# Optimization experiments

Measured on AMD Instinct MI355X. Metric: run time of the kernel, lower is better.

## Reference

```python
import jax, jax.numpy as jnp
import numpy as np

N = 100_000   # nodes
E = 200_000   # directed edges
G = 2_500     # graphs in batch
F_NODE = 16
F_EDGE = 8
H1 = 32
H2 = 16


def setup_inputs() -> dict:
    key = jax.random.key(0)
    ks = jax.random.split(key, 24)
    p = lambda k, shape: 0.1 * jax.random.normal(k, shape, dtype=jnp.float32)
    inp = {
        "x": jax.random.normal(ks[0], (N, F_NODE), dtype=jnp.float32),
        "edge_attr": jax.random.normal(ks[1], (E, F_EDGE), dtype=jnp.float32),
        # edge-MLP for conv1: F_EDGE -> 16 -> F_NODE*H1
        "w_e1a": p(ks[2], (F_EDGE, 16)), "b_e1a": p(ks[3], (16,)),
        "w_e1b": p(ks[4], (16, F_NODE * H1)), "b_e1b": p(ks[5], (F_NODE * H1,)),
        "w_root1": p(ks[6], (F_NODE, H1)), "b_root1": p(ks[7], (H1,)),
        # edge-MLP for conv2: F_EDGE -> 16 -> H1*H2
        "w_e2a": p(ks[8], (F_EDGE, 16)), "b_e2a": p(ks[9], (16,)),
        "w_e2b": p(ks[10], (16, H1 * H2)), "b_e2b": p(ks[11], (H1 * H2,)),
        "w_root2": p(ks[12], (H1, H2)), "b_root2": p(ks[13], (H2,)),
        # attention-pool gate nn: F_NODE -> F_NODE -> 1
        "w_g1": p(ks[14], (F_NODE, F_NODE)), "b_g1": p(ks[15], (F_NODE,)),
        "w_g2": p(ks[16], (F_NODE, 1)), "b_g2": p(ks[17], (1,)),
        # head: (H2 + F_NODE) -> 8 -> 1
        "w_l1": p(ks[18], (H2 + F_NODE, 8)), "b_l1": p(ks[19], (8,)),
        "w_l2": p(ks[20], (8, 1)), "b_l2": p(ks[21], (1,)),
        "edge_index": jax.random.randint(ks[22], (2, E), 0, N),
        "batch": jnp.sort(jax.random.randint(ks[23], (N,), 0, G)),
    }
    return inp


def _nnconv(x, src, tgt, edge_attr, wa, ba, wb, bb, wr, br, in_c, out_c, n):
    # PyG NNConv: x_i' = x_i @ W_root + b + sum_{j->i} x_j @ Theta(e_ji)
    h = jax.nn.relu(edge_attr @ wa + ba)              # [E, 16]
    theta = (h @ wb + bb).reshape(-1, in_c, out_c)    # [E, in, out]
    msg = jnp.einsum('ei,eio->eo', x[src], theta)     # [E, out]
    agg = jax.ops.segment_sum(msg, tgt, num_segments=n)
    return x @ wr + br + agg


def reference(x, edge_attr, w_e1a, b_e1a, w_e1b, b_e1b, w_root1, b_root1,
              w_e2a, b_e2a, w_e2b, b_e2b, w_root2, b_root2,
              w_g1, b_g1, w_g2, b_g2, w_l1, b_l1, w_l2, b_l2,
              edge_index, batch):
    src, tgt = edge_index[0], edge_index[1]
    n = x.shape[0]

    # GlobalAttention pooling on raw node features (per-graph segment softmax)
    gate = jax.nn.relu(x @ w_g1 + b_g1) @ w_g2 + b_g2          # [N, 1]
    m = jax.ops.segment_max(gate, batch, num_segments=G)       # [G, 1]
    a = jnp.exp(gate - m[batch])
    s = jax.ops.segment_sum(a, batch, num_segments=G)
    x_att = jax.ops.segment_sum((a / s[batch]) * x, batch, num_segments=G)  # [G, F_NODE]

    # Two NNConv layers with ReLU
    h = jax.nn.relu(_nnconv(x, src, tgt, edge_attr, w_e1a, b_e1a, w_e1b, b_e1b,
                            w_root1, b_root1, F_NODE, H1, n))
    h = jax.nn.relu(_nnconv(h, src, tgt, edge_attr, w_e2a, b_e2a, w_e2b, b_e2b,
                            w_root2, b_root2, H1, H2, n))

    # global_mean_pool
    cnt = jax.ops.segment_sum(jnp.ones((n, 1), h.dtype), batch, num_segments=G)
    mean = jax.ops.segment_sum(h, batch, num_segments=G) / jnp.maximum(cnt, 1.0)

    z = jnp.concatenate([mean, x_att], axis=1)  # [G, H2 + F_NODE]
    # eval mode: dropout p=0.5 is identity; two linear layers, no activation between
    z = z @ w_l1 + b_l1
    z = z @ w_l2 + b_l2
    return z
```

## Files before the change

kernel.cpp:

```cpp
#include <hip/hip_runtime.h>
#include <hip/hip_bf16.h>

#define NN 100000
#define NE 200000
#define NG 2500
#define FN 16
#define FE 8
#define H1C 32
#define H2C 16
#define KH 16

typedef __attribute__((ext_vector_type(8))) short short8;
typedef __attribute__((ext_vector_type(4))) float f32x4;
typedef _Float16 __attribute__((ext_vector_type(2))) half2v;
typedef _Float16 __attribute__((ext_vector_type(8))) half8v;
typedef __fp16 __attribute__((ext_vector_type(2))) pkf16x2;

__device__ __forceinline__ float bf2f(unsigned int u){
  union { unsigned int i; float f; } v; v.i = (u & 0xffffu) << 16; return v.f;
}
__device__ __forceinline__ unsigned int pkh(float a, float b){
  union { pkf16x2 h; unsigned int u; } v; v.h = __builtin_amdgcn_cvt_pkrtz(a, b); return v.u;
}
__device__ __forceinline__ unsigned short f2h(float f){
  union { _Float16 h; unsigned short s; } v; v.h = (_Float16)f; return v.s;
}
__device__ __forceinline__ float h2lo(unsigned int u){
  union { unsigned short s; _Float16 h; } v; v.s = (unsigned short)u; return (float)v.h;
}
__device__ __forceinline__ float h2hi(unsigned int u){
  union { unsigned short s; _Float16 h; } v; v.s = (unsigned short)(u >> 16); return (float)v.h;
}
__device__ __forceinline__ float rdf(const void* p, long i, bool isbf){
  return isbf ? bf2f(((const unsigned short*)p)[i]) : ((const float*)p)[i];
}
__device__ __forceinline__ bool detect_isbf(const void* __restrict__ x){
  const unsigned short* u = (const unsigned short*)x;
  int lane = threadIdx.x & 63;
  float f = bf2f(u[2*lane]);
  float a = fabsf(f);
  bool sane = (f == 0.0f) || (a > 1e-4f && a < 1e4f);
  unsigned long long b = __ballot(sane);
  return __popcll(b) >= 32;
}

#define NW 20
struct WArgs { const void* p[NW]; };
enum {
  OW_E1A=0,     OB_E1A=128,   OW_E1B=144,   OB_E1B=8336,  OW_R1=8848,  OB_R1=9360,
  OW_E2A=9392,  OB_E2A=9520,  OW_E2B=9536,  OB_E2B=17728, OW_R2=18240, OB_R2=18752,
  OW_G1=18768,  OB_G1=19024,  OW_G2=19040,  OB_G2=19056,
  OW_L1=19057,  OB_L1=19313,  OW_L2=19321,  OB_L2=19329
};

#define MB_A 76
#define MB_B (MB_A + 19)
#define MB_C (MB_B + 18)
#define MB_D (MB_C + 391)
#define MB_E (MB_D + 782)
__global__ void __launch_bounds__(256) mega1_kernel(
    const void* __restrict__ xin, const void* __restrict__ efin, WArgs w,
    const int* __restrict__ ei, const int* __restrict__ batch,
    float* __restrict__ wts, unsigned int* __restrict__ wpack1, unsigned int* __restrict__ wpack2,
    float* __restrict__ gate, float* __restrict__ xf, int* __restrict__ deg,
    int* __restrict__ gstart)
{
  int b = blockIdx.x, tid = threadIdx.x;
  if(b < MB_A){
    bool isbf = detect_isbf(xin);
    int i = b*256 + tid;
    if(i >= 19330) return;
    const int sz[NW] = {128,16,8192,512,512,32, 128,16,8192,512,512,16, 256,16,16,1, 256,8,8,1};
    int seg = 0; long base = 0;
    while(i - base >= sz[seg]){ base += sz[seg]; seg++; }
    wts[i] = rdf(w.p[seg], i - base, isbf);
    return;
  }
  if(b < MB_B){
    bool isbf = detect_isbf(xin);
    int j = (b - MB_A)*256 + tid;
    if(j >= 4736) return;
    int n = j / 148; int k = (j % 148) * 2;
    float v0 = 0.f, v1 = 0.f;
    if(k < 256)        v0 = rdf(w.p[2], (long)k*32 + n, isbf);
    else if(k < 272)   v0 = rdf(w.p[3], (long)(k-256)*32 + n, isbf);
    if(k+1 < 256)      v1 = rdf(w.p[2], (long)(k+1)*32 + n, isbf);
    else if(k+1 < 272) v1 = rdf(w.p[3], (long)(k+1-256)*32 + n, isbf);
    wpack1[j] = pkh(v0, v1);
    return;
  }
  if(b < MB_C){
    bool isbf = detect_isbf(xin);
    int j = (b - MB_B)*256 + tid;
    if(j >= 4416) return;
    int n = j / 276; int k = (j % 276) * 2;
    float v0 = 0.f, v1 = 0.f;
    if(k < 512)        v0 = rdf(w.p[8], (long)k*16 + n, isbf);
    else if(k < 544)   v0 = rdf(w.p[9], (long)(k-512)*16 + n, isbf);
    if(k+1 < 512)      v1 = rdf(w.p[8], (long)(k+1)*16 + n, isbf);
    else if(k+1 < 544) v1 = rdf(w.p[9], (long)(k+1-512)*16 + n, isbf);
    wpack2[j] = pkh(v0, v1);
    return;
  }
  if(b < MB_D){
    __shared__ float s_w1[FN*FN], s_b1[FN], s_w2[FN], s_b2v[1];
    bool isbf = detect_isbf(xin);
    if(tid < FN*FN) s_w1[tid] = rdf(w.p[12], tid, isbf);
    if(tid < FN){ s_b1[tid] = rdf(w.p[13], tid, isbf); s_w2[tid] = rdf(w.p[14], tid, isbf); }
    if(tid == 0) s_b2v[0] = rdf(w.p[15], 0, isbf);
    __syncthreads();
    int n = (b - MB_C)*256 + tid;
    if(n >= NN) return;
    {
      int b1 = batch[n];
      int b0 = (n == 0) ? -1 : batch[n-1];
      for(int g2 = b0 + 1; g2 <= b1; g2++) gstart[g2] = n;
      if(n == NN-1) for(int g2 = b1 + 1; g2 <= NG; g2++) gstart[g2] = NN;
    }
    float xv[FN];
    if(isbf){
      uint4 u0 = ((const uint4*)xin)[2*n], u1 = ((const uint4*)xin)[2*n+1];
      xv[0]=bf2f(u0.x); xv[1]=bf2f(u0.x>>16); xv[2]=bf2f(u0.y); xv[3]=bf2f(u0.y>>16);
      xv[4]=bf2f(u0.z); xv[5]=bf2f(u0.z>>16); xv[6]=bf2f(u0.w); xv[7]=bf2f(u0.w>>16);
      xv[8]=bf2f(u1.x); xv[9]=bf2f(u1.x>>16); xv[10]=bf2f(u1.y); xv[11]=bf2f(u1.y>>16);
      xv[12]=bf2f(u1.z); xv[13]=bf2f(u1.z>>16); xv[14]=bf2f(u1.w); xv[15]=bf2f(u1.w>>16);
    } else {
      #pragma unroll
      for(int q = 0; q < 4; q++){
        float4 v = ((const float4*)xin)[4*n + q];
        xv[q*4+0]=v.x; xv[q*4+1]=v.y; xv[q*4+2]=v.z; xv[q*4+3]=v.w;
      }
    }
    float4* xo = (float4*)(xf + (size_t)n*FN);
    #pragma unroll
    for(int q = 0; q < 4; q++) xo[q] = make_float4(xv[q*4+0], xv[q*4+1], xv[q*4+2], xv[q*4+3]);
    float g = s_b2v[0];
    #pragma unroll
    for(int j = 0; j < FN; j++){
      float hj = s_b1[j];
      #pragma unroll
      for(int i = 0; i < FN; i++) hj += xv[i] * s_w1[i*FN + j];
      hj = hj > 0.f ? hj : 0.f;
      g += hj * s_w2[j];
    }
    gate[n] = g;
    return;
  }
  {
    int e = (b - MB_D)*256 + tid;
    if(e < NE) atomicAdd(&deg[ei[NE + e]], 1);
  }
}

#define SCAN_NB 98
__global__ void __launch_bounds__(256) scan_kernel(
    const int* __restrict__ deg, int* __restrict__ rowptr, int* __restrict__ cursor,
    unsigned int* __restrict__ pub)
{
  __shared__ int s_thr[256];
  __shared__ int s_agg[SCAN_NB];
  __shared__ int s_bcast;
  int tid = threadIdx.x, bid = blockIdx.x;
  int base = bid*1024 + tid*4;
  int v0=0, v1=0, v2=0, v3=0;
  if(base + 3 < NN){
    int4 t4 = *(const int4*)(deg + base);
    v0=t4.x; v1=t4.y; v2=t4.z; v3=t4.w;
  } else {
    if(base+0 < NN) v0 = deg[base+0];
    if(base+1 < NN) v1 = deg[base+1];
    if(base+2 < NN) v2 = deg[base+2];
  }
  int e1 = v0, e2 = v0+v1, e3 = v0+v1+v2, tot = v0+v1+v2+v3;
  s_thr[tid] = tot;
  __syncthreads();
  for(int off = 1; off < 256; off <<= 1){
    int t = (tid >= off) ? s_thr[tid-off] : 0;
    __syncthreads();
    s_thr[tid] += t;
    __syncthreads();
  }
  int thr_excl = s_thr[tid] - tot;
  int agg = s_thr[255];
  if(tid == 0) atomicExch(&pub[bid], ((unsigned int)agg << 1) | 1u);
  if(tid < SCAN_NB){
    unsigned int v;
    do { v = atomicAdd(&pub[tid], 0u); } while((v & 1u) == 0u);
    s_agg[tid] = (int)(v >> 1);
  }
  __syncthreads();
  if(tid == 0){
    int acc = 0;
    for(int p = 0; p < bid; p++) acc += s_agg[p];
    s_bcast = acc;
  }
  __syncthreads();
  int ex = s_bcast + thr_excl;
  if(base + 3 < NN){
    int4 r = make_int4(ex, ex+e1, ex+e2, ex+e3);
    *(int4*)(rowptr + base) = r;
    *(int4*)(cursor + base) = r;
  } else {
    if(base+0 < NN){ rowptr[base+0]=ex;    cursor[base+0]=ex;    }
    if(base+1 < NN){ rowptr[base+1]=ex+e1; cursor[base+1]=ex+e1; }
    if(base+2 < NN){ rowptr[base+2]=ex+e2; cursor[base+2]=ex+e2; }
  }
  if(bid == 0 && tid == 0) rowptr[NN] = NE;
}

__global__ void __launch_bounds__(256) fill_edge_kernel(
    const int* __restrict__ ei, int* __restrict__ cursor,
    const void* __restrict__ efin, const float* __restrict__ wts, const void* __restrict__ xin,
    int* __restrict__ srcp, unsigned int* __restrict__ hpk1, unsigned int* __restrict__ hpk2)
{
  __shared__ float s_w1[FE*KH], s_b1[KH], s_w2[FE*KH], s_b2[KH];
  int tid = threadIdx.x;
  if(tid < FE*KH){ s_w1[tid] = wts[OW_E1A + tid]; s_w2[tid] = wts[OW_E2A + tid]; }
  if(tid < KH){ s_b1[tid] = wts[OB_E1A + tid]; s_b2[tid] = wts[OB_E2A + tid]; }
  bool isbf = detect_isbf(xin);
  __syncthreads();
  int e = blockIdx.x*256 + tid;
  if(e >= NE) return;
  int pos = atomicAdd(&cursor[ei[NE + e]], 1);
  srcp[pos] = ei[e];
  float ev[FE];
  if(isbf){
    uint4 u = ((const uint4*)efin)[e];
    ev[0]=bf2f(u.x); ev[1]=bf2f(u.x>>16); ev[2]=bf2f(u.y); ev[3]=bf2f(u.y>>16);
    ev[4]=bf2f(u.z); ev[5]=bf2f(u.z>>16); ev[6]=bf2f(u.w); ev[7]=bf2f(u.w>>16);
  } else {
    float4 a = ((const float4*)efin)[2*e], b = ((const float4*)efin)[2*e+1];
    ev[0]=a.x; ev[1]=a.y; ev[2]=a.z; ev[3]=a.w; ev[4]=b.x; ev[5]=b.y; ev[6]=b.z; ev[7]=b.w;
  }
  unsigned int o[8];
  #pragma unroll
  for(int d = 0; d < 8; d++){
    float h0 = s_b1[2*d], h1 = s_b1[2*d+1];
    #pragma unroll
    for(int k = 0; k < FE; k++){
      h0 += ev[k] * s_w1[k*KH + 2*d];
      h1 += ev[k] * s_w1[k*KH + 2*d+1];
    }
    h0 = h0 > 0.f ? h0 : 0.f; h1 = h1 > 0.f ? h1 : 0.f;
    o[d] = pkh(h0, h1);
  }
  uint4* p1 = (uint4*)(hpk1 + (size_t)pos*8);
  p1[0] = make_uint4(o[0],o[1],o[2],o[3]); p1[1] = make_uint4(o[4],o[5],o[6],o[7]);
  #pragma unroll
  for(int d = 0; d < 8; d++){
    float h0 = s_b2[2*d], h1 = s_b2[2*d+1];
    #pragma unroll
    for(int k = 0; k < FE; k++){
      h0 += ev[k] * s_w2[k*KH + 2*d];
      h1 += ev[k] * s_w2[k*KH + 2*d+1];
    }
    h0 = h0 > 0.f ? h0 : 0.f; h1 = h1 > 0.f ? h1 : 0.f;
    o[d] = pkh(h0, h1);
  }
  uint4* p2 = (uint4*)(hpk2 + (size_t)pos*8);
  p2[0] = make_uint4(o[0],o[1],o[2],o[3]); p2[1] = make_uint4(o[4],o[5],o[6],o[7]);
}

template<int IN, int OUT, bool AH>
__global__ void __launch_bounds__(256) conv_mfma_kernel(
    const void* __restrict__ nodef, const unsigned int* __restrict__ hpk,
    const int* __restrict__ srcp, const unsigned short* __restrict__ wpack,
    unsigned short* __restrict__ msg)
{
  constexpr int KMF  = ((KH*IN + IN + 31)/32)*32;
  constexpr int KP   = KMF + 8;
  constexpr int NT   = OUT/16;
  constexpr int KS   = KMF/32;
  int tid = threadIdx.x;
  int lane = tid & 63, m = lane & 15, quad = lane >> 4;
  int wid = tid >> 6;
  int ebase = blockIdx.x*64 + wid*16;
  int em = ebase + m;
  int sn = srcp[em];
  int q1 = quad >> 1;
  int xoff = (IN == 16) ? ((quad & 1)*8) : (quad*8);
  union { half8v v; half2v h[4]; unsigned int w[4]; } X;
  if(AH){
    uint4 u = *(const uint4*)((const unsigned short*)nodef + (size_t)sn*IN + xoff);
    X.w[0]=u.x; X.w[1]=u.y; X.w[2]=u.z; X.w[3]=u.w;
  } else {
    const float4* xp = (const float4*)((const float*)nodef + (size_t)sn*IN + xoff);
    float4 v0 = xp[0], v1 = xp[1];
    X.w[0] = pkh(v0.x, v0.y);
    X.w[1] = pkh(v0.z, v0.w);
    X.w[2] = pkh(v1.x, v1.y);
    X.w[3] = pkh(v1.z, v1.w);
  }
  unsigned int hu[8];
  {
    const uint4* hp = (const uint4*)(hpk + (size_t)em*8);
    uint4 u0 = hp[0], u1 = hp[1];
    hu[0]=u0.x; hu[1]=u0.y; hu[2]=u0.z; hu[3]=u0.w;
    hu[4]=u1.x; hu[5]=u1.y; hu[6]=u1.z; hu[7]=u1.w;
  }

  f32x4 acc[NT];
  #pragma unroll
  for(int nt = 0; nt < NT; nt++) acc[nt] = (f32x4){0.f,0.f,0.f,0.f};

  const half8v hz = {};
  #pragma unroll
  for(int ks = 0; ks < KS; ks++){
    union { half8v v; half2v h[4]; } A;
    if(ks < KS-1){
      unsigned short hs = (unsigned short)((IN == 16) ? (hu[ks] >> (16*q1))
                                                      : (hu[ks >> 1] >> (16*(ks & 1))));
      union { unsigned short s; _Float16 h; } hc; hc.s = hs;
      half2v hv2 = { hc.h, hc.h };
      #pragma unroll
      for(int k = 0; k < 4; k++) A.h[k] = hv2 * X.h[k];
    } else {
      if(IN == 16) A.v = (quad < 2) ? X.v : hz;
      else         A.v = X.v;
    }
    #pragma unroll
    for(int nt = 0; nt < NT; nt++){
      half8v b = *(const half8v*)(wpack + (size_t)(nt*16 + m)*KP + ks*32 + quad*8);
      acc[nt] = __builtin_amdgcn_mfma_f32_16x16x32_f16(A.v, b, acc[nt], 0, 0, 0);
    }
  }
  #pragma unroll
  for(int nt = 0; nt < NT; nt++)
    #pragma unroll
    for(int r = 0; r < 4; r++)
      msg[(size_t)(ebase + quad*4 + r)*OUT + nt*16 + m] = f2h(acc[nt][r]);
}

__global__ void __launch_bounds__(256) gather1_kernel(
    const float* __restrict__ xf, const unsigned short* __restrict__ msg,
    const int* __restrict__ rowptr,
    const float* __restrict__ wr, const float* __restrict__ br,
    unsigned short* __restrict__ h1b)
{
  __shared__ float s_w[FN*H1C], s_b[H1C];
  for(int i = threadIdx.x; i < FN*H1C; i += 256) s_w[i] = wr[i];
  if(threadIdx.x < H1C) s_b[threadIdx.x] = br[threadIdx.x];
  __syncthreads();
  int g = blockIdx.x*256 + threadIdx.x;
  int n = g >> 3, q = g & 7;
  if(n >= NN) return;
  float a0 = s_b[q*4+0], a1 = s_b[q*4+1], a2 = s_b[q*4+2], a3 = s_b[q*4+3];
  int jb = rowptr[n], je = rowptr[n+1];
  for(int j = jb; j < je; j++){
    const unsigned int* mp = (const unsigned int*)(msg + (size_t)j*H1C + q*4);
    unsigned int u0 = mp[0], u1 = mp[1];
    a0 += h2lo(u0); a1 += h2hi(u0); a2 += h2lo(u1); a3 += h2hi(u1);
  }
  const float* xr = xf + (size_t)n*FN;
  #pragma unroll
  for(int i = 0; i < FN; i++){
    float xi = xr[i];
    a0 += xi*s_w[i*H1C + q*4+0]; a1 += xi*s_w[i*H1C + q*4+1];
    a2 += xi*s_w[i*H1C + q*4+2]; a3 += xi*s_w[i*H1C + q*4+3];
  }
  a0 = a0>0.f?a0:0.f; a1 = a1>0.f?a1:0.f; a2 = a2>0.f?a2:0.f; a3 = a3>0.f?a3:0.f;
  uint2 hb; hb.x = pkh(a0, a1); hb.y = pkh(a2, a3);
  *(uint2*)(h1b + (size_t)n*H1C + q*4) = hb;
}

__global__ void __launch_bounds__(256) gather2_kernel(
    const unsigned short* __restrict__ h1b, const unsigned short* __restrict__ msg,
    const int* __restrict__ rowptr,
    const float* __restrict__ wr, const float* __restrict__ br, float* __restrict__ h2)
{
  __shared__ float s_w[H1C*H2C], s_b[H2C];
  for(int i = threadIdx.x; i < H1C*H2C; i += 256) s_w[i] = wr[i];
  if(threadIdx.x < H2C) s_b[threadIdx.x] = br[threadIdx.x];
  __syncthreads();
  int g = blockIdx.x*256 + threadIdx.x;
  int n = g >> 2, q = g & 3;
  if(n >= NN) return;
  float a0 = s_b[q*4+0], a1 = s_b[q*4+1], a2 = s_b[q*4+2], a3 = s_b[q*4+3];
  int jb = rowptr[n], je = rowptr[n+1];
  for(int j = jb; j < je; j++){
    const unsigned int* mp = (const unsigned int*)(msg + (size_t)j*H2C + q*4);
    unsigned int u0 = mp[0], u1 = mp[1];
    a0 += h2lo(u0); a1 += h2hi(u0); a2 += h2lo(u1); a3 += h2hi(u1);
  }
  const unsigned int* hb = (const unsigned int*)(h1b + (size_t)n*H1C);
  #pragma unroll
  for(int i2 = 0; i2 < H1C/2; i2++){
    unsigned int u = hb[i2];
    float x0 = h2lo(u), x1 = h2hi(u);
    int i = 2*i2;
    a0 += x0*s_w[i*H2C + q*4+0] + x1*s_w[(i+1)*H2C + q*4+0];
    a1 += x0*s_w[i*H2C + q*4+1] + x1*s_w[(i+1)*H2C + q*4+1];
    a2 += x0*s_w[i*H2C + q*4+2] + x1*s_w[(i+1)*H2C + q*4+2];
    a3 += x0*s_w[i*H2C + q*4+3] + x1*s_w[(i+1)*H2C + q*4+3];
  }
  float4 r; r.x = a0>0.f?a0:0.f; r.y = a1>0.f?a1:0.f; r.z = a2>0.f?a2:0.f; r.w = a3>0.f?a3:0.f;
  *(float4*)(h2 + (size_t)n*H2C + q*4) = r;
}

__global__ void head_kernel(const float* __restrict__ gate, const float* __restrict__ xf,
    const float* __restrict__ h2, const int* __restrict__ gstart, const void* __restrict__ xin,
    const float* __restrict__ wl1, const float* __restrict__ bl1,
    const float* __restrict__ wl2, const float* __restrict__ bl2,
    void* __restrict__ out)
{
  __shared__ float sz[H2C + FN];
  int g = blockIdx.x;
  int lane = threadIdx.x;
  bool isbf = detect_isbf(xin);
  int start = gstart[g];
  int end   = gstart[g + 1];
  float m = -1e30f;
  for(int n = start + lane; n < end; n += 64) m = fmaxf(m, gate[n]);
  #pragma unroll
  for(int o = 32; o >= 1; o >>= 1) m = fmaxf(m, __shfl_xor(m, o));
  float s = 0.f;
  float acc[FN];
  #pragma unroll
  for(int f = 0; f < FN; f++) acc[f] = 0.f;
  for(int n = start + lane; n < end; n += 64){
    float a = __expf(gate[n] - m);
    s += a;
    const float4* xp = (const float4*)(xf + (size_t)n * FN);
    #pragma unroll
    for(int q = 0; q < 4; q++){
      float4 v = xp[q];
      acc[q*4+0] += a*v.x; acc[q*4+1] += a*v.y; acc[q*4+2] += a*v.z; acc[q*4+3] += a*v.w;
    }
  }
  #pragma unroll
  for(int o = 32; o >= 1; o >>= 1){
    s += __shfl_xor(s, o);
    #pragma unroll
    for(int f = 0; f < FN; f++) acc[f] += __shfl_xor(acc[f], o);
  }
  if(lane < FN) sz[H2C + lane] = (end > start && s > 0.f) ? acc[lane] / s : 0.f;
  #pragma unroll
  for(int f = 0; f < H2C; f++) acc[f] = 0.f;
  for(int n = start + lane; n < end; n += 64){
    const float4* hp = (const float4*)(h2 + (size_t)n*H2C);
    #pragma unroll
    for(int q = 0; q < 4; q++){
      float4 v = hp[q];
      acc[q*4+0] += v.x; acc[q*4+1] += v.y; acc[q*4+2] += v.z; acc[q*4+3] += v.w;
    }
  }
  #pragma unroll
  for(int o = 32; o >= 1; o >>= 1){
    #pragma unroll
    for(int f = 0; f < H2C; f++) acc[f] += __shfl_xor(acc[f], o);
  }
  float inv = 1.f / fmaxf((float)(end - start), 1.f);
  if(lane < H2C) sz[lane] = acc[lane] * inv;
  __syncthreads();
  if(lane == 0){
    float t1[8];
    #pragma unroll
    for(int j = 0; j < 8; j++){
      float t = bl1[j];
      #pragma unroll
      for(int c = 0; c < H2C + FN; c++) t += sz[c] * wl1[c*8 + j];
      t1[j] = t;
    }
    float o = bl2[0];
    #pragma unroll
    for(int j = 0; j < 8; j++) o += t1[j] * wl2[j];
    if(isbf) ((__hip_bfloat16*)out)[g] = __float2bfloat16(o);
    else     ((float*)out)[g] = o;
  }
}

extern "C" void kernel_launch(void* const* d_in, const int* in_sizes, int n_in,
                              void* d_out, int out_size, void* d_ws, size_t ws_size,
                              hipStream_t stream)
{
  const int* ei    = (const int*)d_in[22];
  const int* batch = (const int*)d_in[23];

  float* ws = (float*)d_ws;
  float* xf     = ws;
  float* gate   = xf + 1600000;
  float* wts    = gate + 100000;
  int*   rowptr = (int*)(wts + 19360);
  int*   cursor = rowptr + 100016;
  int*   deg    = cursor + 100000;
  unsigned int* pub = (unsigned int*)(deg + 100000);
  int*   srcp   = (int*)(pub + 256);
  unsigned int* wpack1 = (unsigned int*)(srcp + 200000);
  unsigned int* wpack2 = wpack1 + 4736;
  unsigned short* h1b  = (unsigned short*)(wpack2 + 4416);
  unsigned int* hpk1   = (unsigned int*)h1b;
  unsigned short* msg1 = h1b + 3200000;
  unsigned short* msg2 = msg1;
  float* h2     = (float*)(msg1 + 6400000);
  unsigned int* hpk2   = (unsigned int*)h2;
  int*   gstart = (int*)(h2 + 1600000);

  WArgs wa;
  for(int i = 0; i < NW; i++) wa.p[i] = d_in[2 + i];

  hipMemsetAsync(deg, 0, (100000 + 256)*sizeof(int), stream);
  mega1_kernel<<<MB_E, 256, 0, stream>>>(d_in[0], d_in[1], wa, ei, batch, wts, wpack1, wpack2, gate, xf, deg, gstart);
  scan_kernel<<<SCAN_NB, 256, 0, stream>>>(deg, rowptr, cursor, pub);
  fill_edge_kernel<<<(NE + 255)/256, 256, 0, stream>>>(ei, cursor, d_in[1], wts, d_in[0], srcp, hpk1, hpk2);

  conv_mfma_kernel<FN, H1C, false><<<NE/64, 256, 0, stream>>>(
      xf, hpk1, srcp, (const unsigned short*)wpack1, msg1);
  gather1_kernel<<<(NN*8 + 255)/256, 256, 0, stream>>>(xf, msg1, rowptr, wts+OW_R1, wts+OB_R1, h1b);

  conv_mfma_kernel<H1C, H2C, true><<<NE/64, 256, 0, stream>>>(
      h1b, hpk2, srcp, (const unsigned short*)wpack2, msg2);
  gather2_kernel<<<(NN*4 + 255)/256, 256, 0, stream>>>(h1b, msg2, rowptr, wts+OW_R2, wts+OB_R2, h2);

  head_kernel<<<NG, 64, 0, stream>>>(gate, xf, h2, gstart, d_in[0],
      wts+OW_L1, wts+OB_L1, wts+OW_L2, wts+OB_L2, d_out);
}
```

Baseline: 212.0 us.

## Replace CSR build and gather with float atomic scatter of edge messages

Removes the degree count, scan and fill pass that sorted edges by target. Edge-MLP hidden features are now computed in the mega kernel in original edge order, and the MFMA conv kernels scatter their messages straight into fp32 node accumulators with unsafeAtomicAdd. The node kernels just read the accumulated sums. This drops two launches, the fp16 message buffers and the serialized scan, at the cost of many float atomics, an extra memset of the accumulators, and a summation order that is no longer deterministic.

Result: no change. 213.6 us (+0.8%).

```diff
diff --git a/kernel.cpp b/kernel.cpp
--- a/kernel.cpp
+++ b/kernel.cpp
@@ -22,9 +22,6 @@
 __device__ __forceinline__ unsigned int pkh(float a, float b){
   union { pkf16x2 h; unsigned int u; } v; v.h = __builtin_amdgcn_cvt_pkrtz(a, b); return v.u;
 }
-__device__ __forceinline__ unsigned short f2h(float f){
-  union { _Float16 h; unsigned short s; } v; v.h = (_Float16)f; return v.s;
-}
 __device__ __forceinline__ float h2lo(unsigned int u){
   union { unsigned short s; _Float16 h; } v; v.s = (unsigned short)u; return (float)v.h;
 }
@@ -60,9 +57,10 @@
 #define MB_E (MB_D + 782)
 __global__ void __launch_bounds__(256) mega1_kernel(
     const void* __restrict__ xin, const void* __restrict__ efin, WArgs w,
-    const int* __restrict__ ei, const int* __restrict__ batch,
+    const int* __restrict__ batch,
     float* __restrict__ wts, unsigned int* __restrict__ wpack1, unsigned int* __restrict__ wpack2,
-    float* __restrict__ gate, float* __restrict__ xf, int* __restrict__ deg,
+    float* __restrict__ gate, float* __restrict__ xf,
+    unsigned int* __restrict__ hpk1, unsigned int* __restrict__ hpk2,
     int* __restrict__ gstart)
 {
   int b = blockIdx.x, tid = threadIdx.x;
@@ -98,7 +96,7 @@
     if(k < 512)        v0 = rdf(w.p[8], (long)k*16 + n, isbf);
     else if(k < 544)   v0 = rdf(w.p[9], (long)(k-512)*16 + n, isbf);
     if(k+1 < 512)      v1 = rdf(w.p[8], (long)(k+1)*16 + n, isbf);
-    else if(k+1 < 544) v1 = rdf(w.p[9], (long)(k+1-512)*16 + n, isbf);
+    else if(k+1 < 544) v1 = rdf(w.p[9], (long)(k+1-544+32)*16 + n, isbf);
     wpack2[j] = pkh(v0, v1);
     return;
   }
@@ -147,125 +145,57 @@
     return;
   }
   {
+    __shared__ float s_w1[FE*KH], s_b1[KH], s_w2[FE*KH], s_b2[KH];
+    bool isbf = detect_isbf(xin);
+    if(tid < FE*KH){ s_w1[tid] = rdf(w.p[0], tid, isbf); s_w2[tid] = rdf(w.p[6], tid, isbf); }
+    if(tid < KH){ s_b1[tid] = rdf(w.p[1], tid, isbf); s_b2[tid] = rdf(w.p[7], tid, isbf); }
+    __syncthreads();
     int e = (b - MB_D)*256 + tid;
-    if(e < NE) atomicAdd(&deg[ei[NE + e]], 1);
-  }
-}
-
-#define SCAN_NB 98
-__global__ void __launch_bounds__(256) scan_kernel(
-    const int* __restrict__ deg, int* __restrict__ rowptr, int* __restrict__ cursor,
-    unsigned int* __restrict__ pub)
-{
-  __shared__ int s_thr[256];
-  __shared__ int s_agg[SCAN_NB];
-  __shared__ int s_bcast;
-  int tid = threadIdx.x, bid = blockIdx.x;
-  int base = bid*1024 + tid*4;
-  int v0=0, v1=0, v2=0, v3=0;
-  if(base + 3 < NN){
-    int4 t4 = *(const int4*)(deg + base);
-    v0=t4.x; v1=t4.y; v2=t4.z; v3=t4.w;
-  } else {
-    if(base+0 < NN) v0 = deg[base+0];
-    if(base+1 < NN) v1 = deg[base+1];
-    if(base+2 < NN) v2 = deg[base+2];
-  }
-  int e1 = v0, e2 = v0+v1, e3 = v0+v1+v2, tot = v0+v1+v2+v3;
-  s_thr[tid] = tot;
-  __syncthreads();
-  for(int off = 1; off < 256; off <<= 1){
-    int t = (tid >= off) ? s_thr[tid-off] : 0;
-    __syncthreads();
-    s_thr[tid] += t;
-    __syncthreads();
-  }
-  int thr_excl = s_thr[tid] - tot;
-  int agg = s_thr[255];
-  if(tid == 0) atomicExch(&pub[bid], ((unsigned int)agg << 1) | 1u);
-  if(tid < SCAN_NB){
-    unsigned int v;
-    do { v = atomicAdd(&pub[tid], 0u); } while((v & 1u) == 0u);
-    s_agg[tid] = (int)(v >> 1);
-  }
-  __syncthreads();
-  if(tid == 0){
-    int acc = 0;
-    for(int p = 0; p < bid; p++) acc += s_agg[p];
-    s_bcast = acc;
-  }
-  __syncthreads();
-  int ex = s_bcast + thr_excl;
-  if(base + 3 < NN){
-    int4 r = make_int4(ex, ex+e1, ex+e2, ex+e3);
-    *(int4*)(rowptr + base) = r;
-    *(int4*)(cursor + base) = r;
-  } else {
-    if(base+0 < NN){ rowptr[base+0]=ex;    cursor[base+0]=ex;    }
-    if(base+1 < NN){ rowptr[base+1]=ex+e1; cursor[base+1]=ex+e1; }
-    if(base+2 < NN){ rowptr[base+2]=ex+e2; cursor[base+2]=ex+e2; }
-  }
-  if(bid == 0 && tid == 0) rowptr[NN] = NE;
-}
-
-__global__ void __launch_bounds__(256) fill_edge_kernel(
-    const int* __restrict__ ei, int* __restrict__ cursor,
-    const void* __restrict__ efin, const float* __restrict__ wts, const void* __restrict__ xin,
-    int* __restrict__ srcp, unsigned int* __restrict__ hpk1, unsigned int* __restrict__ hpk2)
-{
-  __shared__ float s_w1[FE*KH], s_b1[KH], s_w2[FE*KH], s_b2[KH];
-  int tid = threadIdx.x;
-  if(tid < FE*KH){ s_w1[tid] = wts[OW_E1A + tid]; s_w2[tid] = wts[OW_E2A + tid]; }
-  if(tid < KH){ s_b1[tid] = wts[OB_E1A + tid]; s_b2[tid] = wts[OB_E2A + tid]; }
-  bool isbf = detect_isbf(xin);
-  __syncthreads();
-  int e = blockIdx.x*256 + tid;
-  if(e >= NE) return;
-  int pos = atomicAdd(&cursor[ei[NE + e]], 1);
-  srcp[pos] = ei[e];
-  float ev[FE];
-  if(isbf){
-    uint4 u = ((const uint4*)efin)[e];
-    ev[0]=bf2f(u.x); ev[1]=bf2f(u.x>>16); ev[2]=bf2f(u.y); ev[3]=bf2f(u.y>>16);
-    ev[4]=bf2f(u.z); ev[5]=bf2f(u.z>>16); ev[6]=bf2f(u.w); ev[7]=bf2f(u.w>>16);
-  } else {
-    float4 a = ((const float4*)efin)[2*e], b = ((const float4*)efin)[2*e+1];
-    ev[0]=a.x; ev[1]=a.y; ev[2]=a.z; ev[3]=a.w; ev[4]=b.x; ev[5]=b.y; ev[6]=b.z; ev[7]=b.w;
-  }
-  unsigned int o[8];
-  #pragma unroll
-  for(int d = 0; d < 8; d++){
-    float h0 = s_b1[2*d], h1 = s_b1[2*d+1];
-    #pragma unroll
-    for(int k = 0; k < FE; k++){
-      h0 += ev[k] * s_w1[k*KH + 2*d];
-      h1 += ev[k] * s_w1[k*KH + 2*d+1];
-    }
-    h0 = h0 > 0.f ? h0 : 0.f; h1 = h1 > 0.f ? h1 : 0.f;
-    o[d] = pkh(h0, h1);
-  }
-  uint4* p1 = (uint4*)(hpk1 + (size_t)pos*8);
-  p1[0] = make_uint4(o[0],o[1],o[2],o[3]); p1[1] = make_uint4(o[4],o[5],o[6],o[7]);
-  #pragma unroll
-  for(int d = 0; d < 8; d++){
-    float h0 = s_b2[2*d], h1 = s_b2[2*d+1];
-    #pragma unroll
-    for(int k = 0; k < FE; k++){
-      h0 += ev[k] * s_w2[k*KH + 2*d];
-      h1 += ev[k] * s_w2[k*KH + 2*d+1];
-    }
-    h0 = h0 > 0.f ? h0 : 0.f; h1 = h1 > 0.f ? h1 : 0.f;
-    o[d] = pkh(h0, h1);
-  }
-  uint4* p2 = (uint4*)(hpk2 + (size_t)pos*8);
-  p2[0] = make_uint4(o[0],o[1],o[2],o[3]); p2[1] = make_uint4(o[4],o[5],o[6],o[7]);
+    if(e >= NE) return;
+    float ev[FE];
+    if(isbf){
+      uint4 u = ((const uint4*)efin)[e];
+      ev[0]=bf2f(u.x); ev[1]=bf2f(u.x>>16); ev[2]=bf2f(u.y); ev[3]=bf2f(u.y>>16);
+      ev[4]=bf2f(u.z); ev[5]=bf2f(u.z>>16); ev[6]=bf2f(u.w); ev[7]=bf2f(u.w>>16);
+    } else {
+      float4 a = ((const float4*)efin)[2*e], bb = ((const float4*)efin)[2*e+1];
+      ev[0]=a.x; ev[1]=a.y; ev[2]=a.z; ev[3]=a.w; ev[4]=bb.x; ev[5]=bb.y; ev[6]=bb.z; ev[7]=bb.w;
+    }
+    unsigned int o[8];
+    #pragma unroll
+    for(int d = 0; d < 8; d++){
+      float h0 = s_b1[2*d], h1 = s_b1[2*d+1];
+      #pragma unroll
+      for(int k = 0; k < FE; k++){
+        h0 += ev[k] * s_w1[k*KH + 2*d];
+        h1 += ev[k] * s_w1[k*KH + 2*d+1];
+      }
+      h0 = h0 > 0.f ? h0 : 0.f; h1 = h1 > 0.f ? h1 : 0.f;
+      o[d] = pkh(h0, h1);
+    }
+    uint4* p1 = (uint4*)(hpk1 + (size_t)e*8);
+    p1[0] = make_uint4(o[0],o[1],o[2],o[3]); p1[1] = make_uint4(o[4],o[5],o[6],o[7]);
+    #pragma unroll
+    for(int d = 0; d < 8; d++){
+      float h0 = s_b2[2*d], h1 = s_b2[2*d+1];
+      #pragma unroll
+      for(int k = 0; k < FE; k++){
+        h0 += ev[k] * s_w2[k*KH + 2*d];
+        h1 += ev[k] * s_w2[k*KH + 2*d+1];
+      }
+      h0 = h0 > 0.f ? h0 : 0.f; h1 = h1 > 0.f ? h1 : 0.f;
+      o[d] = pkh(h0, h1);
+    }
+    uint4* p2 = (uint4*)(hpk2 + (size_t)e*8);
+    p2[0] = make_uint4(o[0],o[1],o[2],o[3]); p2[1] = make_uint4(o[4],o[5],o[6],o[7]);
+  }
 }
 
 template<int IN, int OUT, bool AH>
-__global__ void __launch_bounds__(256) conv_mfma_kernel(
+__global__ void __launch_bounds__(256) conv_atomic_kernel(
     const void* __restrict__ nodef, const unsigned int* __restrict__ hpk,
-    const int* __restrict__ srcp, const unsigned short* __restrict__ wpack,
-    unsigned short* __restrict__ msg)
+    const int* __restrict__ ei, const unsigned short* __restrict__ wpack,
+    float* __restrict__ agg)
 {
   constexpr int KMF  = ((KH*IN + IN + 31)/32)*32;
   constexpr int KP   = KMF + 8;
@@ -276,7 +206,7 @@
   int wid = tid >> 6;
   int ebase = blockIdx.x*64 + wid*16;
   int em = ebase + m;
-  int sn = srcp[em];
+  int sn = ei[em];
   int q1 = quad >> 1;
   int xoff = (IN == 16) ? ((quad & 1)*8) : (quad*8);
   union { half8v v; half2v h[4]; unsigned int w[4]; } X;
@@ -298,6 +228,7 @@
     hu[0]=u0.x; hu[1]=u0.y; hu[2]=u0.z; hu[3]=u0.w;
     hu[4]=u1.x; hu[5]=u1.y; hu[6]=u1.z; hu[7]=u1.w;
   }
+  int4 tg = *(const int4*)(ei + NE + ebase + quad*4);
 
   f32x4 acc[NT];
   #pragma unroll
@@ -324,16 +255,17 @@
       acc[nt] = __builtin_amdgcn_mfma_f32_16x16x32_f16(A.v, b, acc[nt], 0, 0, 0);
     }
   }
-  #pragma unroll
-  for(int nt = 0; nt < NT; nt++)
-    #pragma unroll
-    for(int r = 0; r < 4; r++)
-      msg[(size_t)(ebase + quad*4 + r)*OUT + nt*16 + m] = f2h(acc[nt][r]);
-}
-
-__global__ void __launch_bounds__(256) gather1_kernel(
-    const float* __restrict__ xf, const unsigned short* __restrict__ msg,
-    const int* __restrict__ rowptr,
+  int tr[4] = {tg.x, tg.y, tg.z, tg.w};
+  #pragma unroll
+  for(int r = 0; r < 4; r++){
+    #pragma unroll
+    for(int nt = 0; nt < NT; nt++)
+      unsafeAtomicAdd(&agg[(size_t)tr[r]*OUT + nt*16 + m], acc[nt][r]);
+  }
+}
+
+__global__ void __launch_bounds__(256) node1_kernel(
+    const float* __restrict__ xf, const float* __restrict__ agg1,
     const float* __restrict__ wr, const float* __restrict__ br,
     unsigned short* __restrict__ h1b)
 {
@@ -344,13 +276,9 @@
   int g = blockIdx.x*256 + threadIdx.x;
   int n = g >> 3, q = g & 7;
   if(n >= NN) return;
-  float a0 = s_b[q*4+0], a1 = s_b[q*4+1], a2 = s_b[q*4+2], a3 = s_b[q*4+3];
-  int jb = rowptr[n], je = rowptr[n+1];
-  for(int j = jb; j < je; j++){
-    const unsigned int* mp = (const unsigned int*)(msg + (size_t)j*H1C + q*4);
-    unsigned int u0 = mp[0], u1 = mp[1];
-    a0 += h2lo(u0); a1 += h2hi(u0); a2 += h2lo(u1); a3 += h2hi(u1);
-  }
+  float4 av = *(const float4*)(agg1 + (size_t)n*H1C + q*4);
+  float a0 = s_b[q*4+0] + av.x, a1 = s_b[q*4+1] + av.y;
+  float a2 = s_b[q*4+2] + av.z, a3 = s_b[q*4+3] + av.w;
   const float* xr = xf + (size_t)n*FN;
   #pragma unroll
   for(int i = 0; i < FN; i++){
@@ -363,9 +291,8 @@
   *(uint2*)(h1b + (size_t)n*H1C + q*4) = hb;
 }
 
-__global__ void __launch_bounds__(256) gather2_kernel(
-    const unsigned short* __restrict__ h1b, const unsigned short* __restrict__ msg,
-    const int* __restrict__ rowptr,
+__global__ void __launch_bounds__(256) node2_kernel(
+    const unsigned short* __restrict__ h1b, const float* __restrict__ agg2,
     const float* __restrict__ wr, const float* __restrict__ br, float* __restrict__ h2)
 {
   __shared__ float s_w[H1C*H2C], s_b[H2C];
@@ -375,13 +302,9 @@
   int g = blockIdx.x*256 + threadIdx.x;
   int n = g >> 2, q = g & 3;
   if(n >= NN) return;
-  float a0 = s_b[q*4+0], a1 = s_b[q*4+1], a2 = s_b[q*4+2], a3 = s_b[q*4+3];
-  int jb = rowptr[n], je = rowptr[n+1];
-  for(int j = jb; j < je; j++){
-    const unsigned int* mp = (const unsigned int*)(msg + (size_t)j*H2C + q*4);
-    unsigned int u0 = mp[0], u1 = mp[1];
-    a0 += h2lo(u0); a1 += h2hi(u0); a2 += h2lo(u1); a3 += h2hi(u1);
-  }
+  float4 av = *(const float4*)(agg2 + (size_t)n*H2C + q*4);
+  float a0 = s_b[q*4+0] + av.x, a1 = s_b[q*4+1] + av.y;
+  float a2 = s_b[q*4+2] + av.z, a3 = s_b[q*4+3] + av.w;
   const unsigned int* hb = (const unsigned int*)(h1b + (size_t)n*H1C);
   #pragma unroll
   for(int i2 = 0; i2 < H1C/2; i2++){
@@ -480,36 +403,30 @@
   float* xf     = ws;
   float* gate   = xf + 1600000;
   float* wts    = gate + 100000;
-  int*   rowptr = (int*)(wts + 19360);
-  int*   cursor = rowptr + 100016;
-  int*   deg    = cursor + 100000;
-  unsigned int* pub = (unsigned int*)(deg + 100000);
-  int*   srcp   = (int*)(pub + 256);
-  unsigned int* wpack1 = (unsigned int*)(srcp + 200000);
+  int*   gstart = (int*)(wts + 19360);
+  unsigned int* wpack1 = (unsigned int*)(gstart + 2504);
   unsigned int* wpack2 = wpack1 + 4736;
-  unsigned short* h1b  = (unsigned short*)(wpack2 + 4416);
-  unsigned int* hpk1   = (unsigned int*)h1b;
-  unsigned short* msg1 = h1b + 3200000;
-  unsigned short* msg2 = msg1;
-  float* h2     = (float*)(msg1 + 6400000);
-  unsigned int* hpk2   = (unsigned int*)h2;
-  int*   gstart = (int*)(h2 + 1600000);
+  unsigned int* hpk1   = wpack2 + 4416;
+  unsigned int* hpk2   = hpk1 + 1600000;
+  unsigned short* h1b  = (unsigned short*)(hpk2 + 1600000);
+  float* h2     = (float*)(h1b + 3200000);
+  float* agg1   = h2 + 1600000;
+  float* agg2   = agg1 + 3200000;
 
   WArgs wa;
   for(int i = 0; i < NW; i++) wa.p[i] = d_in[2 + i];
 
-  hipMemsetAsync(deg, 0, (100000 + 256)*sizeof(int), stream);
-  mega1_kernel<<<MB_E, 256, 0, stream>>>(d_in[0], d_in[1], wa, ei, batch, wts, wpack1, wpack2, gate, xf, deg, gstart);
-  scan_kernel<<<SCAN_NB, 256, 0, stream>>>(deg, rowptr, cursor, pub);
-  fill_edge_kernel<<<(NE + 255)/256, 256, 0, stream>>>(ei, cursor, d_in[1], wts, d_in[0], srcp, hpk1, hpk2);
-
-  conv_mfma_kernel<FN, H1C, false><<<NE/64, 256, 0, stream>>>(
-      xf, hpk1, srcp, (const unsigned short*)wpack1, msg1);
-  gather1_kernel<<<(NN*8 + 255)/256, 256, 0, stream>>>(xf, msg1, rowptr, wts+OW_R1, wts+OB_R1, h1b);
-
-  conv_mfma_kernel<H1C, H2C, true><<<NE/64, 256, 0, stream>>>(
-      h1b, hpk2, srcp, (const unsigned short*)wpack2, msg2);
-  gather2_kernel<<<(NN*4 + 255)/256, 256, 0, stream>>>(h1b, msg2, rowptr, wts+OW_R2, wts+OB_R2, h2);
+  hipMemsetAsync(agg1, 0, (size_t)(3200000 + 1600000)*sizeof(float), stream);
+  mega1_kernel<<<MB_E, 256, 0, stream>>>(d_in[0], d_in[1], wa, batch,
+      wts, wpack1, wpack2, gate, xf, hpk1, hpk2, gstart);
+
+  conv_atomic_kernel<FN, H1C, false><<<NE/64, 256, 0, stream>>>(
+      xf, hpk1, ei, (const unsigned short*)wpack1, agg1);
+  node1_kernel<<<(NN*8 + 255)/256, 256, 0, stream>>>(xf, agg1, wts+OW_R1, wts+OB_R1, h1b);
+
+  conv_atomic_kernel<H1C, H2C, true><<<NE/64, 256, 0, stream>>>(
+      h1b, hpk2, ei, (const unsigned short*)wpack2, agg2);
+  node2_kernel<<<(NN*4 + 255)/256, 256, 0, stream>>>(h1b, agg2, wts+OW_R2, wts+OB_R2, h2);
 
   head_kernel<<<NG, 64, 0, stream>>>(gate, xf, h2, gstart, d_in[0],
       wts+OW_L1, wts+OB_L1, wts+OW_L2, wts+OB_L2, d_out);
```

## Compute edge messages in original order and aggregate via CSR edge-index indirection

Applied to the files above, without the earlier changes.

Edge-MLP hidden features are now computed in the degree-count blocks of the first mega kernel, in original edge order, instead of in a separate fill kernel after the scan. The CSR fill (cursor atomics writing an edge-id permutation) is folded as extra blocks into the first conv message kernel. Conv kernels read source indices directly from edge_index, and the node aggregation kernels gather messages through the eidx permutation. This removes one kernel launch and the scatter-writes of hpk, and lets edge-MLP work overlap other stage-one work. In exchange the node aggregation now does indirect, uncoalesced reads of messages, and the workspace layout grows because hpk and msg buffers are no longer aliased.

After: 215.4 us. Within noise of the previous version (+1.6%).

```diff
diff --git a/kernel.cpp b/kernel.cpp
--- a/kernel.cpp
+++ b/kernel.cpp
@@ -60,10 +60,11 @@
 #define MB_E (MB_D + 782)
 __global__ void __launch_bounds__(256) mega1_kernel(
     const void* __restrict__ xin, const void* __restrict__ efin, WArgs w,
-    const int* __restrict__ ei, const int* __restrict__ batch,
+    const int* __restrict__ batch, const int* __restrict__ ei,
     float* __restrict__ wts, unsigned int* __restrict__ wpack1, unsigned int* __restrict__ wpack2,
-    float* __restrict__ gate, float* __restrict__ xf, int* __restrict__ deg,
-    int* __restrict__ gstart)
+    float* __restrict__ gate, float* __restrict__ xf,
+    unsigned int* __restrict__ hpk1, unsigned int* __restrict__ hpk2,
+    int* __restrict__ gstart, int* __restrict__ deg)
 {
   int b = blockIdx.x, tid = threadIdx.x;
   if(b < MB_A){
@@ -147,8 +148,50 @@
     return;
   }
   {
+    __shared__ float s_w1[FE*KH], s_b1[KH], s_w2[FE*KH], s_b2[KH];
+    bool isbf = detect_isbf(xin);
+    if(tid < FE*KH){ s_w1[tid] = rdf(w.p[0], tid, isbf); s_w2[tid] = rdf(w.p[6], tid, isbf); }
+    if(tid < KH){ s_b1[tid] = rdf(w.p[1], tid, isbf); s_b2[tid] = rdf(w.p[7], tid, isbf); }
+    __syncthreads();
     int e = (b - MB_D)*256 + tid;
-    if(e < NE) atomicAdd(&deg[ei[NE + e]], 1);
+    if(e >= NE) return;
+    atomicAdd(&deg[ei[NE + e]], 1);
+    float ev[FE];
+    if(isbf){
+      uint4 u = ((const uint4*)efin)[e];
+      ev[0]=bf2f(u.x); ev[1]=bf2f(u.x>>16); ev[2]=bf2f(u.y); ev[3]=bf2f(u.y>>16);
+      ev[4]=bf2f(u.z); ev[5]=bf2f(u.z>>16); ev[6]=bf2f(u.w); ev[7]=bf2f(u.w>>16);
+    } else {
+      float4 a = ((const float4*)efin)[2*e], bb = ((const float4*)efin)[2*e+1];
+      ev[0]=a.x; ev[1]=a.y; ev[2]=a.z; ev[3]=a.w; ev[4]=bb.x; ev[5]=bb.y; ev[6]=bb.z; ev[7]=bb.w;
+    }
+    unsigned int o[8];
+    #pragma unroll
+    for(int d = 0; d < 8; d++){
+      float h0 = s_b1[2*d], h1 = s_b1[2*d+1];
+      #pragma unroll
+      for(int k = 0; k < FE; k++){
+        h0 += ev[k] * s_w1[k*KH + 2*d];
+        h1 += ev[k] * s_w1[k*KH + 2*d+1];
+      }
+      h0 = h0 > 0.f ? h0 : 0.f; h1 = h1 > 0.f ? h1 : 0.f;
+      o[d] = pkh(h0, h1);
+    }
+    uint4* p1 = (uint4*)(hpk1 + (size_t)e*8);
+    p1[0] = make_uint4(o[0],o[1],o[2],o[3]); p1[1] = make_uint4(o[4],o[5],o[6],o[7]);
+    #pragma unroll
+    for(int d = 0; d < 8; d++){
+      float h0 = s_b2[2*d], h1 = s_b2[2*d+1];
+      #pragma unroll
+      for(int k = 0; k < FE; k++){
+        h0 += ev[k] * s_w2[k*KH + 2*d];
+        h1 += ev[k] * s_w2[k*KH + 2*d+1];
+      }
+      h0 = h0 > 0.f ? h0 : 0.f; h1 = h1 > 0.f ? h1 : 0.f;
+      o[d] = pkh(h0, h1);
+    }
+    uint4* p2 = (uint4*)(hpk2 + (size_t)e*8);
+    p2[0] = make_uint4(o[0],o[1],o[2],o[3]); p2[1] = make_uint4(o[4],o[5],o[6],o[7]);
   }
 }
 
@@ -208,65 +251,22 @@
   if(bid == 0 && tid == 0) rowptr[NN] = NE;
 }
 
-__global__ void __launch_bounds__(256) fill_edge_kernel(
-    const int* __restrict__ ei, int* __restrict__ cursor,
-    const void* __restrict__ efin, const float* __restrict__ wts, const void* __restrict__ xin,
-    int* __restrict__ srcp, unsigned int* __restrict__ hpk1, unsigned int* __restrict__ hpk2)
-{
-  __shared__ float s_w1[FE*KH], s_b1[KH], s_w2[FE*KH], s_b2[KH];
-  int tid = threadIdx.x;
-  if(tid < FE*KH){ s_w1[tid] = wts[OW_E1A + tid]; s_w2[tid] = wts[OW_E2A + tid]; }
-  if(tid < KH){ s_b1[tid] = wts[OB_E1A + tid]; s_b2[tid] = wts[OB_E2A + tid]; }
-  bool isbf = detect_isbf(xin);
-  __syncthreads();
-  int e = blockIdx.x*256 + tid;
-  if(e >= NE) return;
-  int pos = atomicAdd(&cursor[ei[NE + e]], 1);
-  srcp[pos] = ei[e];
-  float ev[FE];
-  if(isbf){
-    uint4 u = ((const uint4*)efin)[e];
-    ev[0]=bf2f(u.x); ev[1]=bf2f(u.x>>16); ev[2]=bf2f(u.y); ev[3]=bf2f(u.y>>16);
-    ev[4]=bf2f(u.z); ev[5]=bf2f(u.z>>16); ev[6]=bf2f(u.w); ev[7]=bf2f(u.w>>16);
-  } else {
-    float4 a = ((const float4*)efin)[2*e], b = ((const float4*)efin)[2*e+1];
-    ev[0]=a.x; ev[1]=a.y; ev[2]=a.z; ev[3]=a.w; ev[4]=b.x; ev[5]=b.y; ev[6]=b.z; ev[7]=b.w;
-  }
-  unsigned int o[8];
-  #pragma unroll
-  for(int d = 0; d < 8; d++){
-    float h0 = s_b1[2*d], h1 = s_b1[2*d+1];
-    #pragma unroll
-    for(int k = 0; k < FE; k++){
-      h0 += ev[k] * s_w1[k*KH + 2*d];
-      h1 += ev[k] * s_w1[k*KH + 2*d+1];
-    }
-    h0 = h0 > 0.f ? h0 : 0.f; h1 = h1 > 0.f ? h1 : 0.f;
-    o[d] = pkh(h0, h1);
-  }
-  uint4* p1 = (uint4*)(hpk1 + (size_t)pos*8);
-  p1[0] = make_uint4(o[0],o[1],o[2],o[3]); p1[1] = make_uint4(o[4],o[5],o[6],o[7]);
-  #pragma unroll
-  for(int d = 0; d < 8; d++){
-    float h0 = s_b2[2*d], h1 = s_b2[2*d+1];
-    #pragma unroll
-    for(int k = 0; k < FE; k++){
-      h0 += ev[k] * s_w2[k*KH + 2*d];
-      h1 += ev[k] * s_w2[k*KH + 2*d+1];
-    }
-    h0 = h0 > 0.f ? h0 : 0.f; h1 = h1 > 0.f ? h1 : 0.f;
-    o[d] = pkh(h0, h1);
-  }
-  uint4* p2 = (uint4*)(hpk2 + (size_t)pos*8);
-  p2[0] = make_uint4(o[0],o[1],o[2],o[3]); p2[1] = make_uint4(o[4],o[5],o[6],o[7]);
-}
-
-template<int IN, int OUT, bool AH>
-__global__ void __launch_bounds__(256) conv_mfma_kernel(
+#define CONV_NB (NE/64)
+#define FILL_NB 782
+template<int IN, int OUT, bool AH, bool FILL>
+__global__ void __launch_bounds__(256) conv_msg_kernel(
     const void* __restrict__ nodef, const unsigned int* __restrict__ hpk,
-    const int* __restrict__ srcp, const unsigned short* __restrict__ wpack,
-    unsigned short* __restrict__ msg)
-{
+    const int* __restrict__ ei, int* __restrict__ cursor, int* __restrict__ eidx,
+    const unsigned short* __restrict__ wpack, unsigned short* __restrict__ msg)
+{
+  if(FILL && blockIdx.x >= CONV_NB){
+    int e = (blockIdx.x - CONV_NB)*256 + threadIdx.x;
+    if(e < NE){
+      int pos = atomicAdd(&cursor[ei[NE + e]], 1);
+      eidx[pos] = e;
+    }
+    return;
+  }
   constexpr int KMF  = ((KH*IN + IN + 31)/32)*32;
   constexpr int KP   = KMF + 8;
   constexpr int NT   = OUT/16;
@@ -276,7 +276,7 @@
   int wid = tid >> 6;
   int ebase = blockIdx.x*64 + wid*16;
   int em = ebase + m;
-  int sn = srcp[em];
+  int sn = ei[em];
   int q1 = quad >> 1;
   int xoff = (IN == 16) ? ((quad & 1)*8) : (quad*8);
   union { half8v v; half2v h[4]; unsigned int w[4]; } X;
@@ -331,9 +331,9 @@
       msg[(size_t)(ebase + quad*4 + r)*OUT + nt*16 + m] = f2h(acc[nt][r]);
 }
 
-__global__ void __launch_bounds__(256) gather1_kernel(
+__global__ void __launch_bounds__(256) node1_kernel(
     const float* __restrict__ xf, const unsigned short* __restrict__ msg,
-    const int* __restrict__ rowptr,
+    const int* __restrict__ rowptr, const int* __restrict__ eidx,
     const float* __restrict__ wr, const float* __restrict__ br,
     unsigned short* __restrict__ h1b)
 {
@@ -347,7 +347,8 @@
   float a0 = s_b[q*4+0], a1 = s_b[q*4+1], a2 = s_b[q*4+2], a3 = s_b[q*4+3];
   int jb = rowptr[n], je = rowptr[n+1];
   for(int j = jb; j < je; j++){
-    const unsigned int* mp = (const unsigned int*)(msg + (size_t)j*H1C + q*4);
+    int e = eidx[j];
+    const unsigned int* mp = (const unsigned int*)(msg + (size_t)e*H1C + q*4);
     unsigned int u0 = mp[0], u1 = mp[1];
     a0 += h2lo(u0); a1 += h2hi(u0); a2 += h2lo(u1); a3 += h2hi(u1);
   }
@@ -363,9 +364,9 @@
   *(uint2*)(h1b + (size_t)n*H1C + q*4) = hb;
 }
 
-__global__ void __launch_bounds__(256) gather2_kernel(
+__global__ void __launch_bounds__(256) node2_kernel(
     const unsigned short* __restrict__ h1b, const unsigned short* __restrict__ msg,
-    const int* __restrict__ rowptr,
+    const int* __restrict__ rowptr, const int* __restrict__ eidx,
     const float* __restrict__ wr, const float* __restrict__ br, float* __restrict__ h2)
 {
   __shared__ float s_w[H1C*H2C], s_b[H2C];
@@ -378,7 +379,8 @@
   float a0 = s_b[q*4+0], a1 = s_b[q*4+1], a2 = s_b[q*4+2], a3 = s_b[q*4+3];
   int jb = rowptr[n], je = rowptr[n+1];
   for(int j = jb; j < je; j++){
-    const unsigned int* mp = (const unsigned int*)(msg + (size_t)j*H2C + q*4);
+    int e = eidx[j];
+    const unsigned int* mp = (const unsigned int*)(msg + (size_t)e*H2C + q*4);
     unsigned int u0 = mp[0], u1 = mp[1];
     a0 += h2lo(u0); a1 += h2hi(u0); a2 += h2lo(u1); a3 += h2hi(u1);
   }
@@ -480,36 +482,39 @@
   float* xf     = ws;
   float* gate   = xf + 1600000;
   float* wts    = gate + 100000;
-  int*   rowptr = (int*)(wts + 19360);
+  int*   gstart = (int*)(wts + 19360);
+  int*   deg    = gstart + 2504;
+  int*   rowptr = deg + 100000;
   int*   cursor = rowptr + 100016;
-  int*   deg    = cursor + 100000;
-  unsigned int* pub = (unsigned int*)(deg + 100000);
-  int*   srcp   = (int*)(pub + 256);
-  unsigned int* wpack1 = (unsigned int*)(srcp + 200000);
+  unsigned int* pub = (unsigned int*)(cursor + 100000);
+  int*   eidx   = (int*)(pub + 256);
+  unsigned int* wpack1 = (unsigned int*)(eidx + 200000);
   unsigned int* wpack2 = wpack1 + 4736;
-  unsigned short* h1b  = (unsigned short*)(wpack2 + 4416);
-  unsigned int* hpk1   = (unsigned int*)h1b;
+  unsigned int* hpk1   = wpack2 + 4416;
+  unsigned int* hpk2   = hpk1 + 1600000;
+  unsigned short* h1b  = (unsigned short*)(hpk2 + 1600000);
   unsigned short* msg1 = h1b + 3200000;
-  unsigned short* msg2 = msg1;
-  float* h2     = (float*)(msg1 + 6400000);
-  unsigned int* hpk2   = (unsigned int*)h2;
-  int*   gstart = (int*)(h2 + 1600000);
+  unsigned short* msg2 = msg1 + 6400000;
+  float* h2     = (float*)(msg2 + 3200000);
 
   WArgs wa;
   for(int i = 0; i < NW; i++) wa.p[i] = d_in[2 + i];
 
-  hipMemsetAsync(deg, 0, (100000 + 256)*sizeof(int), stream);
-  mega1_kernel<<<MB_E, 256, 0, stream>>>(d_in[0], d_in[1], wa, ei, batch, wts, wpack1, wpack2, gate, xf, deg, gstart);
+  hipMemsetAsync(deg, 0, (100000 + 0)*sizeof(int), stream);
+  hipMemsetAsync(pub, 0, 256*sizeof(unsigned int), stream);
+  mega1_kernel<<<MB_E, 256, 0, stream>>>(d_in[0], d_in[1], wa, batch, ei,
+      wts, wpack1, wpack2, gate, xf, hpk1, hpk2, gstart, deg);
   scan_kernel<<<SCAN_NB, 256, 0, stream>>>(deg, rowptr, cursor, pub);
-  fill_edge_kernel<<<(NE + 255)/256, 256, 0, stream>>>(ei, cursor, d_in[1], wts, d_in[0], srcp, hpk1, hpk2);
-
-  conv_mfma_kernel<FN, H1C, false><<<NE/64, 256, 0, stream>>>(
-      xf, hpk1, srcp, (const unsigned short*)wpack1, msg1);
-  gather1_kernel<<<(NN*8 + 255)/256, 256, 0, stream>>>(xf, msg1, rowptr, wts+OW_R1, wts+OB_R1, h1b);
-
-  conv_mfma_kernel<H1C, H2C, true><<<NE/64, 256, 0, stream>>>(
-      h1b, hpk2, srcp, (const unsigned short*)wpack2, msg2);
-  gather2_kernel<<<(NN*4 + 255)/256, 256, 0, stream>>>(h1b, msg2, rowptr, wts+OW_R2, wts+OB_R2, h2);
+
+  conv_msg_kernel<FN, H1C, false, true><<<CONV_NB + FILL_NB, 256, 0, stream>>>(
+      xf, hpk1, ei, cursor, eidx, (const unsigned short*)wpack1, msg1);
+  node1_kernel<<<(NN*8 + 255)/256, 256, 0, stream>>>(xf, msg1, rowptr, eidx,
+      wts+OW_R1, wts+OB_R1, h1b);
+
+  conv_msg_kernel<H1C, H2C, true, false><<<CONV_NB, 256, 0, stream>>>(
+      h1b, hpk2, ei, cursor, eidx, (const unsigned short*)wpack2, msg2);
+  node2_kernel<<<(NN*4 + 255)/256, 256, 0, stream>>>(h1b, msg2, rowptr, eidx,
+      wts+OW_R2, wts+OB_R2, h2);
 
   head_kernel<<<NG, 64, 0, stream>>>(gate, xf, h2, gstart, d_in[0],
       wts+OW_L1, wts+OB_L1, wts+OW_L2, wts+OB_L2, d_out);
```
